# Kernel tuning notes

Measured on AMD Instinct MI355X. Metric: run time of the kernel, lower is better.

Reference implementation:

```python
import jax, jax.numpy as jnp
import numpy as np

B, N, D = 8, 8192, 512
HID_ATT = D // 8          # input_dim // num_heads = 64
TOPK = max(1, int(N * 0.3))  # 2457


def _mlp2(x, W1, b1, W2, b2):
    # 2-layer MLP: Linear -> GELU -> Linear (inference mode: dropout/norm off)
    h = jax.nn.gelu(x @ W1 + b1)
    return h @ W2 + b2


def setup_inputs() -> dict:
    key = jax.random.key(0)
    ks = jax.random.split(key, 9)
    s = lambda k, sh, fan: jax.random.normal(k, sh, jnp.float32) * (1.0 / np.sqrt(fan))
    return {
        "x": jax.random.normal(ks[0], (B, N, D), jnp.float32),
        # attention-score MLP: D -> HID_ATT -> 1
        "aW1": s(ks[1], (D, HID_ATT), D),
        "ab1": jnp.zeros((HID_ATT,), jnp.float32),
        "aW2": s(ks[2], (HID_ATT, 1), HID_ATT),
        "ab2": jnp.zeros((1,), jnp.float32),
        # projection MLP: D -> D -> D
        "pW1": s(ks[3], (D, D), D),
        "pb1": jnp.zeros((D,), jnp.float32),
        "pW2": s(ks[4], (D, D), D),
        "pb2": jnp.zeros((D,), jnp.float32),
    }


def reference(x, aW1, ab1, aW2, ab2, pW1, pb1, pW2, pb2):
    # per-instance attention score -> sigmoid weight, [B, N]
    weights = jax.nn.sigmoid(_mlp2(x, aW1, ab1, aW2, ab2)[..., 0])
    # top-k per bag (largest)
    topk_scores, topk_idx = jax.lax.top_k(weights, TOPK)  # [B, TOPK]
    # gather selected instances, scale by score, mean over selected -> [B, D]
    sel = jnp.take_along_axis(x, topk_idx[..., None], axis=1)  # [B, TOPK, D]
    emb = jnp.mean(sel * topk_scores[..., None], axis=1)       # [B, D]
    projection = _mlp2(emb, pW1, pb1, pW2, pb2)                # [B, D]
    return projection, weights
```

## Files before the change

kernel.cpp:

```cpp
#include <hip/hip_runtime.h>
#include <math.h>

#define B_BAGS 8
#define N_INST 8192
#define D_DIM  512
#define H_ATT  64
#define TOPK_K 2457
#define ROWS_TOTAL (B_BAGS * N_INST)

typedef __attribute__((ext_vector_type(8))) short bf16x8;
typedef __attribute__((ext_vector_type(4))) float f32x4;

#define WS_W1P_HI 0
#define WS_W1P_LO 65536
#define WS_PART3  131584
#define WS_PART1  (WS_PART3 + 8*64*512*4)

__device__ __forceinline__ unsigned short bf16_rn(float f) {
  unsigned int x = __float_as_uint(f);
  unsigned int r = (x + 0x7FFFu + ((x >> 16) & 1u)) >> 16;
  return (unsigned short)r;
}
__device__ __forceinline__ float bf16_f(unsigned short u) {
  return __uint_as_float(((unsigned int)u) << 16);
}
__device__ __forceinline__ float gelu_f(float v) {
  float u = 0.7978845608028654f * (v + 0.044715f * v * v * v);
  return 0.5f * v * (1.0f + tanhf(u));
}

__device__ __forceinline__ void cvt_hilo(const float4 u, const float4 v,
                                         bf16x8& h, bf16x8& l) {
  float f[8] = {u.x, u.y, u.z, u.w, v.x, v.y, v.z, v.w};
#pragma unroll
  for (int i = 0; i < 8; i++) {
    unsigned int b = __float_as_uint(f[i]);
    unsigned int hb = b & 0xFFFF0000u;
    float r = f[i] - __uint_as_float(hb);
    h[i] = (short)(b >> 16);
    l[i] = (short)(__float_as_uint(r) >> 16);
  }
}

__device__ __forceinline__ void load_lds16(const void* g, void* l) {
  __builtin_amdgcn_global_load_lds(
      (const __attribute__((address_space(1))) void*)g,
      (__attribute__((address_space(3))) void*)l, 16, 0, 0);
}

__global__ __launch_bounds__(256) void k_prep(const float* __restrict__ aW1,
                                              unsigned short* __restrict__ hi,
                                              unsigned short* __restrict__ lo) {
  int tau = blockIdx.x * 256 + threadIdx.x;
  if (tau >= 4096) return;
  int ks = tau >> 8, t = (tau >> 6) & 3, lane = tau & 63;
  int n = t * 16 + (lane & 15);
  int kb = ks * 32 + (lane >> 4) * 8;
#pragma unroll
  for (int j = 0; j < 8; j++) {
    float v = aW1[(kb + j) * H_ATT + n];
    unsigned short h = bf16_rn(v);
    unsigned short l = bf16_rn(v - bf16_f(h));
    hi[tau * 8 + j] = h;
    lo[tau * 8 + j] = l;
  }
}

#define BM 64
#define AUNIT 1040

__global__ __launch_bounds__(256) void k_scores(
    const float* __restrict__ x,
    const unsigned short* __restrict__ w1p_hi,
    const unsigned short* __restrict__ w1p_lo,
    const float* __restrict__ ab1, const float* __restrict__ aW2,
    const float* __restrict__ ab2, float* __restrict__ wout) {
  __shared__ __align__(16) char Asm[16 * AUNIT];
  __shared__ __align__(16) char Bh[8192];
  __shared__ __align__(16) char Bl[8192];

  int tid = threadIdx.x;
  int wave = tid >> 6, lane = tid & 63;
  int c0 = lane & 15, quad = lane >> 4;
  int rowBase0 = blockIdx.x * BM;

  f32x4 acc[4];
#pragma unroll
  for (int t = 0; t < 4; t++) acc[t] = (f32x4){0.f, 0.f, 0.f, 0.f};

  const int r = wave * 16 + c0;
  const int uA = r >> 2;
  const int aoff = uA * AUNIT + (r & 3) * 256 + quad * 32;

  for (int c = 0; c < 8; c++) {
    size_t kb = (size_t)c * 256;
#pragma unroll
    for (int i = 0; i < 4; i++) {
      int u = wave * 4 + i;
      const char* g = (const char*)x +
          (size_t)(rowBase0 + u * 4 + (lane >> 4)) * 2048 + kb + (size_t)(lane & 15) * 16;
      load_lds16(g, Asm + u * AUNIT);
    }
#pragma unroll
    for (int i = 0; i < 4; i++) {
      int v = wave * 4 + i;
      int vv = v & 7;
      const char* gsrc = (v < 8) ? (const char*)w1p_hi : (const char*)w1p_lo;
      char* ldst = (v < 8) ? Bh : Bl;
      load_lds16(gsrc + (size_t)c * 8192 + vv * 1024 + (size_t)lane * 16,
                 ldst + vv * 1024);
    }
    __syncthreads();

#pragma unroll
    for (int stp = 0; stp < 2; stp++) {
      const float4 a0v = *reinterpret_cast<const float4*>(Asm + aoff + stp * 128);
      const float4 a1v = *reinterpret_cast<const float4*>(Asm + aoff + stp * 128 + 16);
      bf16x8 afh, afl;
      cvt_hilo(a0v, a1v, afh, afl);
      bf16x8 bfh[4], bfl[4];
#pragma unroll
      for (int t = 0; t < 4; t++) {
        bfh[t] = *reinterpret_cast<const bf16x8*>(Bh + (stp * 4 + t) * 1024 + lane * 16);
        bfl[t] = *reinterpret_cast<const bf16x8*>(Bl + (stp * 4 + t) * 1024 + lane * 16);
      }
#pragma unroll
      for (int t = 0; t < 4; t++) {
        acc[t] = __builtin_amdgcn_mfma_f32_16x16x32_bf16(afl, bfh[t], acc[t], 0, 0, 0);
        acc[t] = __builtin_amdgcn_mfma_f32_16x16x32_bf16(afh, bfl[t], acc[t], 0, 0, 0);
        acc[t] = __builtin_amdgcn_mfma_f32_16x16x32_bf16(afh, bfh[t], acc[t], 0, 0, 0);
      }
    }
    __syncthreads();
  }

  float w2v[4], b1v[4];
#pragma unroll
  for (int t = 0; t < 4; t++) {
    w2v[t] = aW2[t * 16 + c0];
    b1v[t] = ab1[t * 16 + c0];
  }
  float bias2 = ab2[0];
  float p[4] = {0.f, 0.f, 0.f, 0.f};
#pragma unroll
  for (int t = 0; t < 4; t++)
#pragma unroll
    for (int rr = 0; rr < 4; rr++) {
      float h = gelu_f(acc[t][rr] + b1v[t]);
      p[rr] += h * w2v[t];
    }
#pragma unroll
  for (int off = 1; off < 16; off <<= 1)
#pragma unroll
    for (int rr = 0; rr < 4; rr++) p[rr] += __shfl_xor(p[rr], off, 64);
  if (c0 == 0) {
    int row = rowBase0 + wave * 16 + quad * 4;
#pragma unroll
    for (int rr = 0; rr < 4; rr++) {
      float sc = p[rr] + bias2;
      wout[row + rr] = 1.0f / (1.0f + expf(-sc));
    }
  }
}

__global__ __launch_bounds__(256) void k_gather(const float* __restrict__ x,
                                                const float* __restrict__ wout,
                                                float* __restrict__ part3) {
  int b = blockIdx.x >> 6;
  int blk = blockIdx.x & 63;
  int tid = threadIdx.x;
  const float* w = wout + b * N_INST;

  unsigned int v[32];
#pragma unroll
  for (int j = 0; j < 32; j++) v[j] = __float_as_uint(w[j * 256 + tid]);

  __shared__ int red[2][4];
  int lane = tid & 63, wv = tid >> 6;
  int pb = 0;
  auto blocksum = [&](int c) -> int {
#pragma unroll
    for (int off = 32; off > 0; off >>= 1) c += __shfl_down(c, off, 64);
    if (lane == 0) red[pb][wv] = c;
    __syncthreads();
    int s = red[pb][0] + red[pb][1] + red[pb][2] + red[pb][3];
    pb ^= 1;
    return s;
  };

  unsigned int lo = 0u, hi = 0x3F800001u;
  while (hi - lo > 1u) {
    unsigned int mid = lo + ((hi - lo) >> 1);
    int c = 0;
#pragma unroll
    for (int j = 0; j < 32; j++) c += (v[j] >= mid) ? 1 : 0;
    if (blocksum(c) >= TOPK_K) lo = mid; else hi = mid;
  }
  unsigned int T = lo;
  int c1 = 0;
#pragma unroll
  for (int j = 0; j < 32; j++) c1 += (v[j] > T) ? 1 : 0;
  c1 = blocksum(c1);
  int needed = TOPK_K - c1;
  unsigned int tm = 0;
#pragma unroll
  for (int j = 0; j < 32; j++) tm |= (v[j] == T ? 1u : 0u) << j;
  int lom = -1, him = N_INST - 1;
  while (him - lom > 1) {
    int mid = (lom + him) >> 1;
    unsigned int mask = 0u;
    if (mid >= tid) {
      unsigned int jmax = (unsigned int)(mid - tid) >> 8;
      mask = (2u << jmax) - 1u;
    }
    if (blocksum((int)__popc(tm & mask)) >= needed) him = mid; else lom = mid;
  }
  int Icut = him;

  __shared__ int idxs[128];
  __shared__ float wgts[128];
  __shared__ int wcnt[2];
  __shared__ float4 xfer[128];

  int r = blk * 128 + tid;
  bool sel = false;
  float wvv = 0.f;
  int pos = 0;
  if (tid < 128) {
    wvv = w[r];
    unsigned int wu = __float_as_uint(wvv);
    sel = (wu > T) || (wu == T && r <= Icut);
    unsigned long long m = __ballot(sel);
    pos = __popcll(m & ((1ull << lane) - 1ull));
    if (lane == 0) wcnt[tid >> 6] = __popcll(m);
  }
  __syncthreads();
  int total = wcnt[0] + wcnt[1];
  if (sel) {
    int base = (tid >= 64) ? wcnt[0] : 0;
    idxs[base + pos] = r;
    wgts[base + pos] = wvv;
  }
  __syncthreads();

  int half = tid >> 7;
  int L = tid & 127;
  float4 acc = {0.f, 0.f, 0.f, 0.f};
  const float* xb = x + (size_t)b * N_INST * D_DIM;
  int i2 = total & ~1;
#pragma unroll 4
  for (int i = 0; i < i2; i += 2) {
    int rr = idxs[i + half];
    float ww = wgts[i + half];
    const float4 xv = *reinterpret_cast<const float4*>(xb + (size_t)rr * D_DIM + L * 4);
    acc.x += ww * xv.x; acc.y += ww * xv.y; acc.z += ww * xv.z; acc.w += ww * xv.w;
  }
  if ((total & 1) && half == 0) {
    int rr = idxs[i2];
    float ww = wgts[i2];
    const float4 xv = *reinterpret_cast<const float4*>(xb + (size_t)rr * D_DIM + L * 4);
    acc.x += ww * xv.x; acc.y += ww * xv.y; acc.z += ww * xv.z; acc.w += ww * xv.w;
  }
  if (half == 1) xfer[L] = acc;
  __syncthreads();
  if (half == 0) {
    float4 o = xfer[L];
    acc.x += o.x; acc.y += o.y; acc.z += o.z; acc.w += o.w;
    *reinterpret_cast<float4*>(part3 + (size_t)(b * 64 + blk) * D_DIM + L * 4) = acc;
  }
}

__global__ __launch_bounds__(256) void k_proj1(const float* __restrict__ part3,
                                               const float* __restrict__ pW1,
                                               float* __restrict__ part1,
                                               const float* __restrict__ pb2,
                                               float* __restrict__ out) {
  int jt = blockIdx.x & 7, kt = blockIdx.x >> 3;
  __shared__ float emb_s[512];
  int tid = threadIdx.x;
  int col = tid & 63, bg = tid >> 6;
  if (kt == 0) {
    float bz = pb2[jt * 64 + col];
    out[(bg * 2) * 512 + jt * 64 + col] = bz;
    out[(bg * 2 + 1) * 512 + jt * 64 + col] = bz;
  }
#pragma unroll
  for (int h = 0; h < 2; h++) {
    int vi = tid + h * 256;
    int b = vi >> 6, d0 = vi & 63;
    const float* p = part3 + (size_t)b * 64 * 512 + kt * 64 + d0;
    float e = 0.f;
#pragma unroll 8
    for (int j = 0; j < 64; j++) e += p[j * 512];
    emb_s[vi] = e * (1.0f / TOPK_K);
  }
  __syncthreads();
  float a0 = 0.f, a1 = 0.f;
  const float* wrow = pW1 + (size_t)(kt * 64) * 512 + jt * 64 + col;
#pragma unroll 8
  for (int q = 0; q < 64; q++) {
    float wq = wrow[q * 512];
    a0 += emb_s[(bg * 2) * 64 + q] * wq;
    a1 += emb_s[(bg * 2 + 1) * 64 + q] * wq;
  }
  part1[kt * 4096 + (bg * 2) * 512 + jt * 64 + col] = a0;
  part1[kt * 4096 + (bg * 2 + 1) * 512 + jt * 64 + col] = a1;
}

__global__ __launch_bounds__(256) void k_proj2(const float* __restrict__ part1,
                                               const float* __restrict__ pb1,
                                               const float* __restrict__ pW2,
                                               float* __restrict__ out) {
  int jt = blockIdx.x & 7, kt = blockIdx.x >> 3;
  __shared__ float h_s[512];
  int tid = threadIdx.x;
#pragma unroll
  for (int h = 0; h < 2; h++) {
    int vi = tid + h * 256;
    int b = vi >> 6, j0 = vi & 63;
    int jj = kt * 64 + j0;
    float s = pb1[jj];
#pragma unroll
    for (int p = 0; p < 8; p++) s += part1[p * 4096 + b * 512 + jj];
    h_s[vi] = gelu_f(s);
  }
  __syncthreads();
  int col = tid & 63, bg = tid >> 6;
  float a0 = 0.f, a1 = 0.f;
  const float* wrow = pW2 + (size_t)(kt * 64) * 512 + jt * 64 + col;
#pragma unroll 8
  for (int q = 0; q < 64; q++) {
    float wq = wrow[q * 512];
    a0 += h_s[(bg * 2) * 64 + q] * wq;
    a1 += h_s[(bg * 2 + 1) * 64 + q] * wq;
  }
  atomicAdd(&out[(bg * 2) * 512 + jt * 64 + col], a0);
  atomicAdd(&out[(bg * 2 + 1) * 512 + jt * 64 + col], a1);
}

extern "C" void kernel_launch(void* const* d_in, const int* in_sizes, int n_in,
                              void* d_out, int out_size, void* d_ws, size_t ws_size,
                              hipStream_t stream) {
  (void)in_sizes; (void)n_in; (void)out_size; (void)ws_size;
  const float* x   = (const float*)d_in[0];
  const float* aW1 = (const float*)d_in[1];
  const float* ab1 = (const float*)d_in[2];
  const float* aW2 = (const float*)d_in[3];
  const float* ab2 = (const float*)d_in[4];
  const float* pW1 = (const float*)d_in[5];
  const float* pb1 = (const float*)d_in[6];
  const float* pW2 = (const float*)d_in[7];
  const float* pb2 = (const float*)d_in[8];

  float* out  = (float*)d_out;
  float* wout = out + B_BAGS * D_DIM;

  char* ws = (char*)d_ws;
  unsigned short* w1p_hi = (unsigned short*)(ws + WS_W1P_HI);
  unsigned short* w1p_lo = (unsigned short*)(ws + WS_W1P_LO);
  float* part3 = (float*)(ws + WS_PART3);
  float* part1 = (float*)(ws + WS_PART1);

  k_prep<<<dim3(16), dim3(256), 0, stream>>>(aW1, w1p_hi, w1p_lo);
  k_scores<<<dim3(ROWS_TOTAL / BM), dim3(256), 0, stream>>>(x, w1p_hi, w1p_lo, ab1, aW2, ab2, wout);
  k_gather<<<dim3(B_BAGS * 64), dim3(256), 0, stream>>>(x, wout, part3);
  k_proj1<<<dim3(64), dim3(256), 0, stream>>>(part3, pW1, part1, pb2, out);
  k_proj2<<<dim3(64), dim3(256), 0, stream>>>(part1, pb1, pW2, out);
}
```

Baseline: 259.4 us.

## Fuse all five stages into one persistent cooperative kernel with grid syncs

Replaces the five separate launches (weight prep, score GEMM, top-k gather, two projection layers) with a single cooperative persistent kernel. Grid-wide barriers separate the stages, and each stage loops over its work items with a grid-stride loop. The aim is to remove per-launch overhead and inter-kernel gaps. In exchange, the grid is capped at the occupancy limit (at most 1024 blocks), grid syncs have their own cost, and the combined kernel's register and LDS use may lower occupancy for the score GEMM stage.

```diff
diff --git a/kernel.cpp b/kernel.cpp
--- a/kernel.cpp
+++ b/kernel.cpp
@@ -1,4 +1,5 @@
 #include <hip/hip_runtime.h>
+#include <hip/hip_cooperative_groups.h>
 #include <math.h>
 
 #define B_BAGS 8
@@ -47,6 +48,9 @@
       (const __attribute__((address_space(1))) void*)g,
       (__attribute__((address_space(3))) void*)l, 16, 0, 0);
 }
+
+#define BM 64
+#define AUNIT 1040
 
 __global__ __launch_bounds__(256) void k_prep(const float* __restrict__ aW1,
                                               unsigned short* __restrict__ hi,
@@ -65,9 +69,6 @@
     lo[tau * 8 + j] = l;
   }
 }
-
-#define BM 64
-#define AUNIT 1040
 
 __global__ __launch_bounds__(256) void k_scores(
     const float* __restrict__ x,
@@ -338,6 +339,302 @@
   atomicAdd(&out[(bg * 2 + 1) * 512 + jt * 64 + col], a1);
 }
 
+__global__ __launch_bounds__(256) void k_fused(
+    const float* __restrict__ x,
+    const float* __restrict__ aW1, const float* __restrict__ ab1,
+    const float* __restrict__ aW2, const float* __restrict__ ab2,
+    const float* __restrict__ pW1, const float* __restrict__ pb1,
+    const float* __restrict__ pW2, const float* __restrict__ pb2,
+    float* __restrict__ out, float* __restrict__ wout,
+    unsigned short* __restrict__ w1p_hi, unsigned short* __restrict__ w1p_lo,
+    float* __restrict__ part3, float* __restrict__ part1) {
+  cooperative_groups::grid_group gg = cooperative_groups::this_grid();
+  __shared__ __align__(16) char SMEM[16 * AUNIT + 16384];
+  const int g = (int)gridDim.x;
+  const int tid = threadIdx.x;
+
+  for (int tau = blockIdx.x * 256 + tid; tau < 4096; tau += g * 256) {
+    int ks = tau >> 8, t = (tau >> 6) & 3, lane = tau & 63;
+    int n = t * 16 + (lane & 15);
+    int kb = ks * 32 + (lane >> 4) * 8;
+#pragma unroll
+    for (int j = 0; j < 8; j++) {
+      float v = aW1[(kb + j) * H_ATT + n];
+      unsigned short h = bf16_rn(v);
+      unsigned short l = bf16_rn(v - bf16_f(h));
+      w1p_hi[tau * 8 + j] = h;
+      w1p_lo[tau * 8 + j] = l;
+    }
+  }
+  __threadfence();
+  gg.sync();
+
+  {
+    char* Asm = SMEM;
+    char* Bh = SMEM + 16 * AUNIT;
+    char* Bl = Bh + 8192;
+    int wave = tid >> 6, lane = tid & 63;
+    int c0 = lane & 15, quad = lane >> 4;
+    const int r = wave * 16 + c0;
+    const int uA = r >> 2;
+    const int aoff = uA * AUNIT + (r & 3) * 256 + quad * 32;
+    float w2v[4], b1v[4];
+#pragma unroll
+    for (int t = 0; t < 4; t++) {
+      w2v[t] = aW2[t * 16 + c0];
+      b1v[t] = ab1[t * 16 + c0];
+    }
+    float bias2 = ab2[0];
+
+    for (int rb = blockIdx.x; rb < ROWS_TOTAL / BM; rb += g) {
+      const int rowBase0 = rb * BM;
+      f32x4 acc[4];
+#pragma unroll
+      for (int t = 0; t < 4; t++) acc[t] = (f32x4){0.f, 0.f, 0.f, 0.f};
+
+      for (int c = 0; c < 8; c++) {
+        size_t kb = (size_t)c * 256;
+#pragma unroll
+        for (int i = 0; i < 4; i++) {
+          int u = wave * 4 + i;
+          const char* gp = (const char*)x +
+              (size_t)(rowBase0 + u * 4 + (lane >> 4)) * 2048 + kb + (size_t)(lane & 15) * 16;
+          load_lds16(gp, Asm + u * AUNIT);
+        }
+#pragma unroll
+        for (int i = 0; i < 4; i++) {
+          int v = wave * 4 + i;
+          int vv = v & 7;
+          const char* gsrc = (v < 8) ? (const char*)w1p_hi : (const char*)w1p_lo;
+          char* ldst = (v < 8) ? Bh : Bl;
+          load_lds16(gsrc + (size_t)c * 8192 + vv * 1024 + (size_t)lane * 16,
+                     ldst + vv * 1024);
+        }
+        __syncthreads();
+
+#pragma unroll
+        for (int stp = 0; stp < 2; stp++) {
+          const float4 a0v = *reinterpret_cast<const float4*>(Asm + aoff + stp * 128);
+          const float4 a1v = *reinterpret_cast<const float4*>(Asm + aoff + stp * 128 + 16);
+          bf16x8 afh, afl;
+          cvt_hilo(a0v, a1v, afh, afl);
+          bf16x8 bfh[4], bfl[4];
+#pragma unroll
+          for (int t = 0; t < 4; t++) {
+            bfh[t] = *reinterpret_cast<const bf16x8*>(Bh + (stp * 4 + t) * 1024 + lane * 16);
+            bfl[t] = *reinterpret_cast<const bf16x8*>(Bl + (stp * 4 + t) * 1024 + lane * 16);
+          }
+#pragma unroll
+          for (int t = 0; t < 4; t++) {
+            acc[t] = __builtin_amdgcn_mfma_f32_16x16x32_bf16(afl, bfh[t], acc[t], 0, 0, 0);
+            acc[t] = __builtin_amdgcn_mfma_f32_16x16x32_bf16(afh, bfl[t], acc[t], 0, 0, 0);
+            acc[t] = __builtin_amdgcn_mfma_f32_16x16x32_bf16(afh, bfh[t], acc[t], 0, 0, 0);
+          }
+        }
+        __syncthreads();
+      }
+
+      float p[4] = {0.f, 0.f, 0.f, 0.f};
+#pragma unroll
+      for (int t = 0; t < 4; t++)
+#pragma unroll
+        for (int rr = 0; rr < 4; rr++) {
+          float h = gelu_f(acc[t][rr] + b1v[t]);
+          p[rr] += h * w2v[t];
+        }
+#pragma unroll
+      for (int off = 1; off < 16; off <<= 1)
+#pragma unroll
+        for (int rr = 0; rr < 4; rr++) p[rr] += __shfl_xor(p[rr], off, 64);
+      if (c0 == 0) {
+        int row = rowBase0 + wave * 16 + quad * 4;
+#pragma unroll
+        for (int rr = 0; rr < 4; rr++) {
+          float sc = p[rr] + bias2;
+          wout[row + rr] = 1.0f / (1.0f + expf(-sc));
+        }
+      }
+    }
+  }
+  __threadfence();
+  gg.sync();
+
+  {
+    int (*red)[4] = reinterpret_cast<int(*)[4]>(SMEM);
+    int* wcnt = reinterpret_cast<int*>(SMEM + 32);
+    int* idxs = reinterpret_cast<int*>(SMEM + 48);
+    float* wgts = reinterpret_cast<float*>(SMEM + 560);
+    float4* xfer = reinterpret_cast<float4*>(SMEM + 1072);
+    int lane = tid & 63, wv = tid >> 6;
+
+    for (int gb = blockIdx.x; gb < B_BAGS * 64; gb += g) {
+      int b = gb >> 6, blk = gb & 63;
+      const float* w = wout + b * N_INST;
+
+      unsigned int v[32];
+#pragma unroll
+      for (int j = 0; j < 32; j++) v[j] = __float_as_uint(w[j * 256 + tid]);
+
+      int pb = 0;
+      auto blocksum = [&](int c) -> int {
+#pragma unroll
+        for (int off = 32; off > 0; off >>= 1) c += __shfl_down(c, off, 64);
+        if (lane == 0) red[pb][wv] = c;
+        __syncthreads();
+        int s = red[pb][0] + red[pb][1] + red[pb][2] + red[pb][3];
+        pb ^= 1;
+        return s;
+      };
+
+      unsigned int lo = 0u, hi = 0x3F800001u;
+      while (hi - lo > 1u) {
+        unsigned int mid = lo + ((hi - lo) >> 1);
+        int c = 0;
+#pragma unroll
+        for (int j = 0; j < 32; j++) c += (v[j] >= mid) ? 1 : 0;
+        if (blocksum(c) >= TOPK_K) lo = mid; else hi = mid;
+      }
+      unsigned int T = lo;
+      int c1 = 0;
+#pragma unroll
+      for (int j = 0; j < 32; j++) c1 += (v[j] > T) ? 1 : 0;
+      c1 = blocksum(c1);
+      int needed = TOPK_K - c1;
+      unsigned int tm = 0;
+#pragma unroll
+      for (int j = 0; j < 32; j++) tm |= (v[j] == T ? 1u : 0u) << j;
+      int lom = -1, him = N_INST - 1;
+      while (him - lom > 1) {
+        int mid = (lom + him) >> 1;
+        unsigned int mask = 0u;
+        if (mid >= tid) {
+          unsigned int jmax = (unsigned int)(mid - tid) >> 8;
+          mask = (2u << jmax) - 1u;
+        }
+        if (blocksum((int)__popc(tm & mask)) >= needed) him = mid; else lom = mid;
+      }
+      int Icut = him;
+
+      int r2 = blk * 128 + tid;
+      bool sel = false;
+      float wvv = 0.f;
+      int pos = 0;
+      if (tid < 128) {
+        wvv = w[r2];
+        unsigned int wu = __float_as_uint(wvv);
+        sel = (wu > T) || (wu == T && r2 <= Icut);
+        unsigned long long m = __ballot(sel);
+        pos = __popcll(m & ((1ull << lane) - 1ull));
+        if (lane == 0) wcnt[tid >> 6] = __popcll(m);
+      }
+      __syncthreads();
+      int total = wcnt[0] + wcnt[1];
+      if (sel) {
+        int base = (tid >= 64) ? wcnt[0] : 0;
+        idxs[base + pos] = r2;
+        wgts[base + pos] = wvv;
+      }
+      __syncthreads();
+
+      int half = tid >> 7;
+      int L = tid & 127;
+      float4 acc = {0.f, 0.f, 0.f, 0.f};
+      const float* xb = x + (size_t)b * N_INST * D_DIM;
+      int i2 = total & ~1;
+#pragma unroll 4
+      for (int i = 0; i < i2; i += 2) {
+        int rr = idxs[i + half];
+        float ww = wgts[i + half];
+        const float4 xv = *reinterpret_cast<const float4*>(xb + (size_t)rr * D_DIM + L * 4);
+        acc.x += ww * xv.x; acc.y += ww * xv.y; acc.z += ww * xv.z; acc.w += ww * xv.w;
+      }
+      if ((total & 1) && half == 0) {
+        int rr = idxs[i2];
+        float ww = wgts[i2];
+        const float4 xv = *reinterpret_cast<const float4*>(xb + (size_t)rr * D_DIM + L * 4);
+        acc.x += ww * xv.x; acc.y += ww * xv.y; acc.z += ww * xv.z; acc.w += ww * xv.w;
+      }
+      if (half == 1) xfer[L] = acc;
+      __syncthreads();
+      if (half == 0) {
+        float4 o = xfer[L];
+        acc.x += o.x; acc.y += o.y; acc.z += o.z; acc.w += o.w;
+        *reinterpret_cast<float4*>(part3 + (size_t)(b * 64 + blk) * D_DIM + L * 4) = acc;
+      }
+      __syncthreads();
+    }
+  }
+  __threadfence();
+  gg.sync();
+
+  {
+    float* emb_s = reinterpret_cast<float*>(SMEM);
+    for (int pbk = blockIdx.x; pbk < 64; pbk += g) {
+      int jt = pbk & 7, kt = pbk >> 3;
+      int col = tid & 63, bg = tid >> 6;
+      if (kt == 0) {
+        float bz = pb2[jt * 64 + col];
+        out[(bg * 2) * 512 + jt * 64 + col] = bz;
+        out[(bg * 2 + 1) * 512 + jt * 64 + col] = bz;
+      }
+#pragma unroll
+      for (int h = 0; h < 2; h++) {
+        int vi = tid + h * 256;
+        int b = vi >> 6, d0 = vi & 63;
+        const float* p = part3 + (size_t)b * 64 * 512 + kt * 64 + d0;
+        float e = 0.f;
+#pragma unroll 8
+        for (int j = 0; j < 64; j++) e += p[j * 512];
+        emb_s[vi] = e * (1.0f / TOPK_K);
+      }
+      __syncthreads();
+      float a0 = 0.f, a1 = 0.f;
+      const float* wrow = pW1 + (size_t)(kt * 64) * 512 + jt * 64 + col;
+#pragma unroll 8
+      for (int q = 0; q < 64; q++) {
+        float wq = wrow[q * 512];
+        a0 += emb_s[(bg * 2) * 64 + q] * wq;
+        a1 += emb_s[(bg * 2 + 1) * 64 + q] * wq;
+      }
+      part1[kt * 4096 + (bg * 2) * 512 + jt * 64 + col] = a0;
+      part1[kt * 4096 + (bg * 2 + 1) * 512 + jt * 64 + col] = a1;
+      __syncthreads();
+    }
+  }
+  __threadfence();
+  gg.sync();
+
+  {
+    float* h_s = reinterpret_cast<float*>(SMEM);
+    for (int pbk = blockIdx.x; pbk < 64; pbk += g) {
+      int jt = pbk & 7, kt = pbk >> 3;
+#pragma unroll
+      for (int h = 0; h < 2; h++) {
+        int vi = tid + h * 256;
+        int b = vi >> 6, j0 = vi & 63;
+        int jj = kt * 64 + j0;
+        float s = pb1[jj];
+#pragma unroll
+        for (int p = 0; p < 8; p++) s += part1[p * 4096 + b * 512 + jj];
+        h_s[vi] = gelu_f(s);
+      }
+      __syncthreads();
+      int col = tid & 63, bg = tid >> 6;
+      float a0 = 0.f, a1 = 0.f;
+      const float* wrow = pW2 + (size_t)(kt * 64) * 512 + jt * 64 + col;
+#pragma unroll 8
+      for (int q = 0; q < 64; q++) {
+        float wq = wrow[q * 512];
+        a0 += h_s[(bg * 2) * 64 + q] * wq;
+        a1 += h_s[(bg * 2 + 1) * 64 + q] * wq;
+      }
+      atomicAdd(&out[(bg * 2) * 512 + jt * 64 + col], a0);
+      atomicAdd(&out[(bg * 2 + 1) * 512 + jt * 64 + col], a1);
+      __syncthreads();
+    }
+  }
+}
+
 extern "C" void kernel_launch(void* const* d_in, const int* in_sizes, int n_in,
                               void* d_out, int out_size, void* d_ws, size_t ws_size,
                               hipStream_t stream) {
@@ -361,9 +658,48 @@
   float* part3 = (float*)(ws + WS_PART3);
   float* part1 = (float*)(ws + WS_PART1);
 
-  k_prep<<<dim3(16), dim3(256), 0, stream>>>(aW1, w1p_hi, w1p_lo);
-  k_scores<<<dim3(ROWS_TOTAL / BM), dim3(256), 0, stream>>>(x, w1p_hi, w1p_lo, ab1, aW2, ab2, wout);
-  k_gather<<<dim3(B_BAGS * 64), dim3(256), 0, stream>>>(x, wout, part3);
-  k_proj1<<<dim3(64), dim3(256), 0, stream>>>(part3, pW1, part1, pb2, out);
-  k_proj2<<<dim3(64), dim3(256), 0, stream>>>(part1, pb1, pW2, out);
-}
+  static int coopBlocks = -2;
+  if (coopBlocks == -2) {
+    int dev = 0;
+    hipDeviceProp_t prop;
+    int perCU = 0;
+    if (hipGetDevice(&dev) == hipSuccess &&
+        hipGetDeviceProperties(&prop, dev) == hipSuccess &&
+        prop.cooperativeLaunch &&
+        hipOccupancyMaxActiveBlocksPerMultiprocessor(&perCU, k_fused, 256, 0) ==
+            hipSuccess &&
+        perCU > 0) {
+      long total = (long)perCU * (long)prop.multiProcessorCount;
+      coopBlocks = (int)(total > 1024 ? 1024 : total);
+    } else {
+      coopBlocks = -1;
+    }
+  }
+
+  bool done = false;
+  if (coopBlocks > 0) {
+    void* kargs[] = {
+        (void*)&x, (void*)&aW1, (void*)&ab1, (void*)&aW2, (void*)&ab2,
+        (void*)&pW1, (void*)&pb1, (void*)&pW2, (void*)&pb2,
+        (void*)&out, (void*)&wout, (void*)&w1p_hi, (void*)&w1p_lo,
+        (void*)&part3, (void*)&part1};
+    hipError_t e = hipLaunchCooperativeKernel((const void*)k_fused,
+                                              dim3(coopBlocks), dim3(256),
+                                              kargs, 0, stream);
+    if (e == hipSuccess) {
+      done = true;
+    } else {
+      (void)hipGetLastError();
+      coopBlocks = -1;
+    }
+  }
+
+  if (!done) {
+    k_prep<<<dim3(16), dim3(256), 0, stream>>>(aW1, w1p_hi, w1p_lo);
+    k_scores<<<dim3(ROWS_TOTAL / BM), dim3(256), 0, stream>>>(
+        x, w1p_hi, w1p_lo, ab1, aW2, ab2, wout);
+    k_gather<<<dim3(B_BAGS * 64), dim3(256), 0, stream>>>(x, wout, part3);
+    k_proj1<<<dim3(64), dim3(256), 0, stream>>>(part3, pW1, part1, pb2, out);
+    k_proj2<<<dim3(64), dim3(256), 0, stream>>>(part1, pb1, pW2, out);
+  }
+}
```

Measured after the change: 486.3 us. 1.87x slower.

## Compute top-k threshold once per bag in a separate kernel; split projection K finer

Applied to the files above, without the earlier changes.

The radix-select threshold and tie-break index search move out of k_gather into a new k_thresh kernel. It runs one block per bag and writes the threshold and cut index to workspace. Before, each of the 64 gather blocks per bag recomputed them redundantly. The projection kernels now split the reduction dimension into 16 chunks of 32 instead of 8 of 64, giving 128 blocks each, at the cost of more partial sums to reduce. The extra launch adds serialization and a dependency on the small 8-block threshold kernel.

```diff
diff --git a/kernel.cpp b/kernel.cpp
--- a/kernel.cpp
+++ b/kernel.cpp
@@ -15,6 +15,7 @@
 #define WS_W1P_LO 65536
 #define WS_PART3  131584
 #define WS_PART1  (WS_PART3 + 8*64*512*4)
+#define WS_THRESH (WS_PART1 + 16*8*512*4)
 
 __device__ __forceinline__ unsigned short bf16_rn(float f) {
   unsigned int x = __float_as_uint(f);
@@ -163,11 +164,9 @@
   }
 }
 
-__global__ __launch_bounds__(256) void k_gather(const float* __restrict__ x,
-                                                const float* __restrict__ wout,
-                                                float* __restrict__ part3) {
-  int b = blockIdx.x >> 6;
-  int blk = blockIdx.x & 63;
+__global__ __launch_bounds__(256) void k_thresh(const float* __restrict__ wout,
+                                                unsigned int* __restrict__ thr) {
+  int b = blockIdx.x;
   int tid = threadIdx.x;
   const float* w = wout + b * N_INST;
 
@@ -215,13 +214,30 @@
     }
     if (blocksum((int)__popc(tm & mask)) >= needed) him = mid; else lom = mid;
   }
-  int Icut = him;
+  if (tid == 0) {
+    thr[b * 2] = T;
+    thr[b * 2 + 1] = (unsigned int)him;
+  }
+}
+
+__global__ __launch_bounds__(256) void k_gather(const float* __restrict__ x,
+                                                const float* __restrict__ wout,
+                                                const unsigned int* __restrict__ thr,
+                                                float* __restrict__ part3) {
+  int b = blockIdx.x >> 6;
+  int blk = blockIdx.x & 63;
+  int tid = threadIdx.x;
+  const float* w = wout + b * N_INST;
+
+  unsigned int T = thr[b * 2];
+  int Icut = (int)thr[b * 2 + 1];
 
   __shared__ int idxs[128];
   __shared__ float wgts[128];
   __shared__ int wcnt[2];
   __shared__ float4 xfer[128];
 
+  int lane = tid & 63;
   int r = blk * 128 + tid;
   bool sel = false;
   float wvv = 0.f;
@@ -276,7 +292,7 @@
                                                const float* __restrict__ pb2,
                                                float* __restrict__ out) {
   int jt = blockIdx.x & 7, kt = blockIdx.x >> 3;
-  __shared__ float emb_s[512];
+  __shared__ float emb_s[256];
   int tid = threadIdx.x;
   int col = tid & 63, bg = tid >> 6;
   if (kt == 0) {
@@ -284,24 +300,22 @@
     out[(bg * 2) * 512 + jt * 64 + col] = bz;
     out[(bg * 2 + 1) * 512 + jt * 64 + col] = bz;
   }
-#pragma unroll
-  for (int h = 0; h < 2; h++) {
-    int vi = tid + h * 256;
-    int b = vi >> 6, d0 = vi & 63;
-    const float* p = part3 + (size_t)b * 64 * 512 + kt * 64 + d0;
+  {
+    int b = tid >> 5, d0 = tid & 31;
+    const float* p = part3 + (size_t)b * 64 * 512 + kt * 32 + d0;
     float e = 0.f;
 #pragma unroll 8
     for (int j = 0; j < 64; j++) e += p[j * 512];
-    emb_s[vi] = e * (1.0f / TOPK_K);
+    emb_s[b * 32 + d0] = e * (1.0f / TOPK_K);
   }
   __syncthreads();
   float a0 = 0.f, a1 = 0.f;
-  const float* wrow = pW1 + (size_t)(kt * 64) * 512 + jt * 64 + col;
+  const float* wrow = pW1 + (size_t)(kt * 32) * 512 + jt * 64 + col;
 #pragma unroll 8
-  for (int q = 0; q < 64; q++) {
+  for (int q = 0; q < 32; q++) {
     float wq = wrow[q * 512];
-    a0 += emb_s[(bg * 2) * 64 + q] * wq;
-    a1 += emb_s[(bg * 2 + 1) * 64 + q] * wq;
+    a0 += emb_s[(bg * 2) * 32 + q] * wq;
+    a1 += emb_s[(bg * 2 + 1) * 32 + q] * wq;
   }
   part1[kt * 4096 + (bg * 2) * 512 + jt * 64 + col] = a0;
   part1[kt * 4096 + (bg * 2 + 1) * 512 + jt * 64 + col] = a1;
@@ -312,27 +326,25 @@
                                                const float* __restrict__ pW2,
                                                float* __restrict__ out) {
   int jt = blockIdx.x & 7, kt = blockIdx.x >> 3;
-  __shared__ float h_s[512];
-  int tid = threadIdx.x;
-#pragma unroll
-  for (int h = 0; h < 2; h++) {
-    int vi = tid + h * 256;
-    int b = vi >> 6, j0 = vi & 63;
-    int jj = kt * 64 + j0;
+  __shared__ float h_s[256];
+  int tid = threadIdx.x;
+  {
+    int b = tid >> 5, j0 = tid & 31;
+    int jj = kt * 32 + j0;
     float s = pb1[jj];
 #pragma unroll
-    for (int p = 0; p < 8; p++) s += part1[p * 4096 + b * 512 + jj];
-    h_s[vi] = gelu_f(s);
+    for (int p = 0; p < 16; p++) s += part1[p * 4096 + b * 512 + jj];
+    h_s[b * 32 + j0] = gelu_f(s);
   }
   __syncthreads();
   int col = tid & 63, bg = tid >> 6;
   float a0 = 0.f, a1 = 0.f;
-  const float* wrow = pW2 + (size_t)(kt * 64) * 512 + jt * 64 + col;
+  const float* wrow = pW2 + (size_t)(kt * 32) * 512 + jt * 64 + col;
 #pragma unroll 8
-  for (int q = 0; q < 64; q++) {
+  for (int q = 0; q < 32; q++) {
     float wq = wrow[q * 512];
-    a0 += h_s[(bg * 2) * 64 + q] * wq;
-    a1 += h_s[(bg * 2 + 1) * 64 + q] * wq;
+    a0 += h_s[(bg * 2) * 32 + q] * wq;
+    a1 += h_s[(bg * 2 + 1) * 32 + q] * wq;
   }
   atomicAdd(&out[(bg * 2) * 512 + jt * 64 + col], a0);
   atomicAdd(&out[(bg * 2 + 1) * 512 + jt * 64 + col], a1);
@@ -360,10 +372,12 @@
   unsigned short* w1p_lo = (unsigned short*)(ws + WS_W1P_LO);
   float* part3 = (float*)(ws + WS_PART3);
   float* part1 = (float*)(ws + WS_PART1);
+  unsigned int* thr = (unsigned int*)(ws + WS_THRESH);
 
   k_prep<<<dim3(16), dim3(256), 0, stream>>>(aW1, w1p_hi, w1p_lo);
   k_scores<<<dim3(ROWS_TOTAL / BM), dim3(256), 0, stream>>>(x, w1p_hi, w1p_lo, ab1, aW2, ab2, wout);
-  k_gather<<<dim3(B_BAGS * 64), dim3(256), 0, stream>>>(x, wout, part3);
-  k_proj1<<<dim3(64), dim3(256), 0, stream>>>(part3, pW1, part1, pb2, out);
-  k_proj2<<<dim3(64), dim3(256), 0, stream>>>(part1, pb1, pW2, out);
-}
+  k_thresh<<<dim3(B_BAGS), dim3(256), 0, stream>>>(wout, thr);
+  k_gather<<<dim3(B_BAGS * 64), dim3(256), 0, stream>>>(x, wout, thr, part3);
+  k_proj1<<<dim3(128), dim3(256), 0, stream>>>(part3, pW1, part1, pb2, out);
+  k_proj2<<<dim3(128), dim3(256), 0, stream>>>(part1, pb1, pW2, out);
+}
```

New measurement: 254.7 us, median of 2. About the same (-1.8%).
